# Performance work log

Hardware: AMD Instinct MI355X
Metric: run time of the kernel (lower is better)

Reference implementation:

```python
import jax, jax.numpy as jnp
import numpy as np

N_FQK, N_FV, N_REL, N_VAL, N_KNOW = 512, 256, 128, 64, 256
TOPK_QK, TOPK_V, TOPK_REL, TOPK_VAL = 64, 32, 16, 3
FQK_END = N_FQK
FV_END = N_FQK + N_FV
REL_END = FV_END + N_REL
VAL_END = REL_END + N_VAL
TOTAL = VAL_END + N_KNOW


def setup_inputs() -> dict:
    key = jax.random.key(0)
    k1, k2, k3, k4, k5 = jax.random.split(key, 5)
    B, S, D, DS = 8, 4096, 1024, 64
    x = jax.random.normal(k1, (B, S, D), dtype=jnp.float32)
    importance = jax.random.uniform(k2, (B, S), dtype=jnp.float32)
    proj_w = jax.random.normal(k3, (DS, D), dtype=jnp.float32) * (1.0 / np.sqrt(D))
    proj_b = jax.random.normal(k4, (DS,), dtype=jnp.float32) * 0.01
    neuron_emb = jax.random.normal(k5, (TOTAL, DS), dtype=jnp.float32) * 0.02
    return {"x": x, "importance": importance, "proj_w": proj_w,
            "proj_b": proj_b, "neuron_emb": neuron_emb}


def _topk_sparsify(w, k):
    # keep top-k values per row, zero elsewhere
    vals, idx = jax.lax.top_k(w, k)
    B = w.shape[0]
    sparse = jnp.zeros_like(w).at[jnp.arange(B)[:, None], idx].set(vals)
    return sparse, idx


def reference(x, importance, proj_w, proj_b, neuron_emb):
    # shared projection + normalized neuron embeddings (eval: dropout off,
    # no excitability bonus)
    h = jnp.einsum('bsd,kd->bsk', x, proj_w) + proj_b          # [B,S,d_space]
    emb_n = neuron_emb / jnp.linalg.norm(neuron_emb, axis=-1, keepdims=True)
    all_logits = jnp.einsum('bsk,nk->bsn', h, emb_n)            # [B,S,TOTAL]

    def agg(logits):
        pref = jax.nn.softmax(logits, axis=-1)                  # [B,S,n]
        return jnp.einsum('bs,bsn->bn', importance, pref)

    w_qk = agg(all_logits[..., :FQK_END])
    _, idx_qk = jax.lax.top_k(w_qk, TOPK_QK)
    idx_qk = jnp.sort(idx_qk, axis=-1)

    w_v = agg(all_logits[..., FQK_END:FV_END])
    _, idx_v = jax.lax.top_k(w_v, TOPK_V)
    idx_v = jnp.sort(idx_v, axis=-1)

    rel_logits = all_logits[..., FV_END:REL_END]
    # relational_Q and relational_K use the same logits slice (eval mode)
    rel_dense_Q = agg(rel_logits)
    rel_dense_K = agg(rel_logits)
    rel_Q, _ = _topk_sparsify(rel_dense_Q, TOPK_REL)
    rel_K, _ = _topk_sparsify(rel_dense_K, TOPK_REL)

    val_dense = agg(all_logits[..., REL_END:VAL_END])
    val_w, _ = _topk_sparsify(val_dense, TOPK_VAL)

    return idx_qk, idx_v, rel_Q, rel_K, val_w
```

## Files before the change

kernel.cpp:

```cpp
#include <hip/hip_runtime.h>


typedef short short8 __attribute__((ext_vector_type(8)));
typedef float f32x4 __attribute__((ext_vector_type(4)));

__device__ __forceinline__ unsigned short f32_to_bf16(float f) {
  unsigned u = __float_as_uint(f);
  u += 0x7FFF + ((u >> 16) & 1);
  return (unsigned short)(u >> 16);
}
__device__ __forceinline__ float bf16_to_f32(unsigned short h) {
  return __uint_as_float(((unsigned)h) << 16);
}
__device__ __forceinline__ void split8(const float4& a0, const float4& a1,
                                       short8& hi, short8& lo) {
  float af[8] = {a0.x, a0.y, a0.z, a0.w, a1.x, a1.y, a1.z, a1.w};
#pragma unroll
  for (int j = 0; j < 8; ++j) {
    unsigned short h = f32_to_bf16(af[j]);
    hi[j] = (short)h;
    lo[j] = (short)f32_to_bf16(af[j] - bf16_to_f32(h));
  }
}
#define MFMA(a, b, c) __builtin_amdgcn_mfma_f32_16x16x32_bf16(a, b, c, 0, 0, 0)

__global__ __launch_bounds__(256) void k_prep(const float* __restrict__ pw,
                                              const float* __restrict__ emb,
                                              unsigned short* __restrict__ whi,
                                              unsigned short* __restrict__ wlo,
                                              unsigned short* __restrict__ ehi,
                                              unsigned short* __restrict__ elo,
                                              float* __restrict__ wg) {
  int tid = blockIdx.x * 256 + threadIdx.x;
  if (tid < 7680) wg[tid] = 0.f;
  for (int i = tid; i < 65536; i += gridDim.x * 256) {
    float v = pw[i];
    unsigned short h = f32_to_bf16(v);
    whi[i] = h;
    wlo[i] = f32_to_bf16(v - bf16_to_f32(h));
  }
  int wid = tid >> 6, lane = tid & 63;
  int nw = gridDim.x * 4;
  for (int n = wid; n < 960; n += nw) {
    float v = emb[n * 64 + lane];
    float s = v * v;
#pragma unroll
    for (int off = 1; off < 64; off <<= 1) s += __shfl_xor(s, off);
    float vn = v / sqrtf(s);
    unsigned short h = f32_to_bf16(vn);
    ehi[n * 64 + lane] = h;
    elo[n * 64 + lane] = f32_to_bf16(vn - bf16_to_f32(h));
  }
}

__global__ __launch_bounds__(256) void k_proj(const float* __restrict__ x,
                                              const unsigned short* __restrict__ whi,
                                              const unsigned short* __restrict__ wlo,
                                              const float* __restrict__ pb,
                                              unsigned short* __restrict__ hhi,
                                              unsigned short* __restrict__ hlo) {
  int tid = threadIdx.x, w = tid >> 6, lane = tid & 63;
  int q = lane >> 4, c = lane & 15;
  int m0 = blockIdx.x * 32;
  int nt = w;

  f32x4 acc[2];
  acc[0] = (f32x4){0.f, 0.f, 0.f, 0.f};
  acc[1] = (f32x4){0.f, 0.f, 0.f, 0.f};

  const float* ap0 = x + (size_t)(m0 + c) * 1024 + q * 8;
  const float* ap1 = x + (size_t)(m0 + 16 + c) * 1024 + q * 8;
  float4 a00 = *(const float4*)(ap0), a01 = *(const float4*)(ap0 + 4);
  float4 a10 = *(const float4*)(ap1), a11 = *(const float4*)(ap1 + 4);

  for (int ks = 0; ks < 32; ++ks) {
    float4 n00, n01, n10, n11;
    if (ks < 31) {
      n00 = *(const float4*)(ap0 + (ks + 1) * 32);
      n01 = *(const float4*)(ap0 + (ks + 1) * 32 + 4);
      n10 = *(const float4*)(ap1 + (ks + 1) * 32);
      n11 = *(const float4*)(ap1 + (ks + 1) * 32 + 4);
    }
    size_t boff = (size_t)(nt * 16 + c) * 1024 + ks * 32 + q * 8;
    short8 bhi = *(const short8*)(whi + boff);
    short8 blo = *(const short8*)(wlo + boff);
    short8 ahi[2], alo[2];
    split8(a00, a01, ahi[0], alo[0]);
    split8(a10, a11, ahi[1], alo[1]);
#pragma unroll
    for (int mt = 0; mt < 2; ++mt) {
      acc[mt] = MFMA(ahi[mt], bhi, acc[mt]);
      acc[mt] = MFMA(ahi[mt], blo, acc[mt]);
      acc[mt] = MFMA(alo[mt], bhi, acc[mt]);
    }
    if (ks < 31) { a00 = n00; a01 = n01; a10 = n10; a11 = n11; }
  }

  float bias = pb[nt * 16 + c];
#pragma unroll
  for (int mt = 0; mt < 2; ++mt) {
#pragma unroll
    for (int r = 0; r < 4; ++r) {
      float val = acc[mt][r] + bias;
      int row = m0 + mt * 16 + q * 4 + r;
      unsigned short h = f32_to_bf16(val);
      hhi[(size_t)row * 64 + nt * 16 + c] = h;
      hlo[(size_t)row * 64 + nt * 16 + c] = f32_to_bf16(val - bf16_to_f32(h));
    }
  }
}

__global__ __launch_bounds__(256) void k_agg(const unsigned short* __restrict__ hhi,
                                             const unsigned short* __restrict__ hlo,
                                             const unsigned short* __restrict__ ehi,
                                             const unsigned short* __restrict__ elo,
                                             const float* __restrict__ imp,
                                             float* __restrict__ wg) {
  __shared__ float zpart[4][32][4];
  __shared__ float coefL[32][4];
  int tid = threadIdx.x, w = tid >> 6, lane = tid & 63;
  int q = lane >> 4, c = lane & 15;
  int row0 = blockIdx.x * 32;
  int b = row0 >> 12;

  short8 Ahi[2][2], Alo[2][2];
#pragma unroll
  for (int mt = 0; mt < 2; ++mt)
#pragma unroll
    for (int ks = 0; ks < 2; ++ks) {
      size_t base = (size_t)(row0 + mt * 16 + c) * 64 + ks * 32 + q * 8;
      Ahi[mt][ks] = *(const short8*)(hhi + base);
      Alo[mt][ks] = *(const short8*)(hlo + base);
    }

  f32x4 zacc[2];
  zacc[0] = (f32x4){0.f, 0.f, 0.f, 0.f};
  zacc[1] = (f32x4){0.f, 0.f, 0.f, 0.f};
  int cur_seg = 0;
  for (int i = 0; i < 15; ++i) {
    int nt = w + 4 * i;
    int s = (nt < 32) ? 0 : (nt < 48) ? 1 : (nt < 56) ? 2 : 3;
    if (s != cur_seg) {
#pragma unroll
      for (int mt = 0; mt < 2; ++mt)
#pragma unroll
        for (int r = 0; r < 4; ++r) {
          float v = zacc[mt][r];
          v += __shfl_xor(v, 1); v += __shfl_xor(v, 2);
          v += __shfl_xor(v, 4); v += __shfl_xor(v, 8);
          if (c == 0) zpart[w][mt * 16 + q * 4 + r][cur_seg] = v;
          zacc[mt][r] = 0.f;
        }
      cur_seg = s;
    }
    size_t eb = (size_t)(nt * 16 + c) * 64 + q * 8;
    short8 bhi0 = *(const short8*)(ehi + eb), bhi1 = *(const short8*)(ehi + eb + 32);
    short8 blo0 = *(const short8*)(elo + eb), blo1 = *(const short8*)(elo + eb + 32);
#pragma unroll
    for (int mt = 0; mt < 2; ++mt) {
      f32x4 l = (f32x4){0.f, 0.f, 0.f, 0.f};
      l = MFMA(Ahi[mt][0], bhi0, l); l = MFMA(Ahi[mt][1], bhi1, l);
      l = MFMA(Ahi[mt][0], blo0, l); l = MFMA(Ahi[mt][1], blo1, l);
      l = MFMA(Alo[mt][0], bhi0, l); l = MFMA(Alo[mt][1], bhi1, l);
#pragma unroll
      for (int r = 0; r < 4; ++r) zacc[mt][r] += __expf(l[r]);
    }
  }
#pragma unroll
  for (int mt = 0; mt < 2; ++mt)
#pragma unroll
    for (int r = 0; r < 4; ++r) {
      float v = zacc[mt][r];
      v += __shfl_xor(v, 1); v += __shfl_xor(v, 2);
      v += __shfl_xor(v, 4); v += __shfl_xor(v, 8);
      if (c == 0) zpart[w][mt * 16 + q * 4 + r][cur_seg] = v;
    }
  __syncthreads();
  if (tid < 128) {
    int row = tid & 31, sg = tid >> 5;
    float Z = zpart[0][row][sg] + zpart[1][row][sg] + zpart[2][row][sg] + zpart[3][row][sg];
    coefL[row][sg] = imp[row0 + row] / Z;
  }
  __syncthreads();

  f32x4 cf[2];
  int cs2 = -1;
  for (int i = 0; i < 15; ++i) {
    int nt = w + 4 * i;
    int s = (nt < 32) ? 0 : (nt < 48) ? 1 : (nt < 56) ? 2 : 3;
    if (s != cs2) {
#pragma unroll
      for (int mt = 0; mt < 2; ++mt)
#pragma unroll
        for (int r = 0; r < 4; ++r) cf[mt][r] = coefL[mt * 16 + q * 4 + r][s];
      cs2 = s;
    }
    size_t eb = (size_t)(nt * 16 + c) * 64 + q * 8;
    short8 bhi0 = *(const short8*)(ehi + eb), bhi1 = *(const short8*)(ehi + eb + 32);
    short8 blo0 = *(const short8*)(elo + eb), blo1 = *(const short8*)(elo + eb + 32);
    float wsum = 0.f;
#pragma unroll
    for (int mt = 0; mt < 2; ++mt) {
      f32x4 l = (f32x4){0.f, 0.f, 0.f, 0.f};
      l = MFMA(Ahi[mt][0], bhi0, l); l = MFMA(Ahi[mt][1], bhi1, l);
      l = MFMA(Ahi[mt][0], blo0, l); l = MFMA(Ahi[mt][1], blo1, l);
      l = MFMA(Alo[mt][0], bhi0, l); l = MFMA(Alo[mt][1], bhi1, l);
#pragma unroll
      for (int r = 0; r < 4; ++r) wsum = fmaf(__expf(l[r]), cf[mt][r], wsum);
    }
    wsum += __shfl_xor(wsum, 16);
    wsum += __shfl_xor(wsum, 32);
    if (lane < 16) atomicAdd(&wg[b * 960 + nt * 16 + c], wsum);
  }
}

__global__ __launch_bounds__(256) void k_topk(const float* __restrict__ wg,
                                              float* __restrict__ out) {
  __shared__ float vals[512];
  __shared__ int flags[512];
  int blk = blockIdx.x;
  int b = blk >> 2, t = blk & 3;
  int tid = threadIdx.x;
  const int Ns[4] = {512, 256, 128, 64};
  const int Ks[4] = {64, 32, 16, 3};
  const int Off[4] = {0, 512, 768, 896};
  int N = Ns[t], K = Ks[t], off = Off[t];
  for (int n = tid; n < N; n += 256) vals[n] = wg[b * 960 + off + n];
  __syncthreads();
  for (int n = tid; n < N; n += 256) {
    float v = vals[n];
    int rank = 0;
    for (int m = 0; m < N; ++m) {
      float u = vals[m];
      rank += (u > v || (u == v && m < n)) ? 1 : 0;
    }
    flags[n] = (rank < K) ? 1 : 0;
  }
  __syncthreads();
  if (t <= 1) {
    if (tid < 64) {
      int base = 0;
      for (int ch = 0; ch < N; ch += 64) {
        int n = ch + tid;
        int f = flags[n];
        unsigned long long mask = __ballot(f);
        if (f) {
          int pos = base + __popcll(mask & ((1ull << tid) - 1ull));
          if (t == 0) out[b * 64 + pos] = (float)n;
          else out[512 + b * 32 + pos] = (float)n;
        }
        base += __popcll(mask);
      }
    }
  } else if (t == 2) {
    for (int n = tid; n < 128; n += 256) {
      float v = flags[n] ? vals[n] : 0.f;
      out[768 + b * 128 + n] = v;
      out[1792 + b * 128 + n] = v;
    }
  } else {
    for (int n = tid; n < 64; n += 256) {
      float v = flags[n] ? vals[n] : 0.f;
      out[2816 + b * 64 + n] = v;
    }
  }
}

extern "C" void kernel_launch(void* const* d_in, const int* in_sizes, int n_in,
                              void* d_out, int out_size, void* d_ws, size_t ws_size,
                              hipStream_t stream) {
  const float* x   = (const float*)d_in[0];
  const float* imp = (const float*)d_in[1];
  const float* pw  = (const float*)d_in[2];
  const float* pb  = (const float*)d_in[3];
  const float* emb = (const float*)d_in[4];
  float* out = (float*)d_out;

  char* ws = (char*)d_ws;
  unsigned short* hhi = (unsigned short*)(ws);
  unsigned short* hlo = (unsigned short*)(ws + 4194304);
  unsigned short* whi = (unsigned short*)(ws + 8388608);
  unsigned short* wlo = (unsigned short*)(ws + 8519680);
  unsigned short* ehi = (unsigned short*)(ws + 8650752);
  unsigned short* elo = (unsigned short*)(ws + 8773632);
  float*          wg  = (float*)(ws + 8896512);

  hipLaunchKernelGGL(k_prep, dim3(64), dim3(256), 0, stream, pw, emb, whi, wlo, ehi, elo, wg);
  hipLaunchKernelGGL(k_proj, dim3(1024), dim3(256), 0, stream, x, whi, wlo, pb, hhi, hlo);
  hipLaunchKernelGGL(k_agg,  dim3(1024), dim3(256), 0, stream, hhi, hlo, ehi, elo, imp, wg);
  hipLaunchKernelGGL(k_topk, dim3(32), dim3(256), 0, stream, wg, out);
}
```

Before: 350.7 us.

## Fuse projection and softmax aggregation into one kernel with split-K across waves

Merges the projection GEMM and the softmax/importance aggregation into a single kernel, so the projected activations stay in shared memory as hi/lo bf16 instead of going through a global round trip. Each block now handles 16 rows. Its four waves split the K dimension of the projection and reduce the partial sums through LDS before the aggregation phase. This removes one launch and about 8 MB of intermediate global traffic. In exchange it doubles the block count, which doubles the atomicAdd traffic into wg, and it raises register use from preloading 16 float4 of x per thread.

```diff
diff --git a/kernel.cpp b/kernel.cpp
--- a/kernel.cpp
+++ b/kernel.cpp
@@ -53,161 +53,140 @@
   }
 }
 
-__global__ __launch_bounds__(256) void k_proj(const float* __restrict__ x,
+__global__ __launch_bounds__(256) void k_main(const float* __restrict__ x,
                                               const unsigned short* __restrict__ whi,
                                               const unsigned short* __restrict__ wlo,
                                               const float* __restrict__ pb,
-                                              unsigned short* __restrict__ hhi,
-                                              unsigned short* __restrict__ hlo) {
+                                              const unsigned short* __restrict__ ehi,
+                                              const unsigned short* __restrict__ elo,
+                                              const float* __restrict__ imp,
+                                              float* __restrict__ wg) {
+  __shared__ __align__(16) float cpart[4][16][68];
+  __shared__ __align__(16) unsigned short hsh[16][72];
+  __shared__ __align__(16) unsigned short hsl[16][72];
+  __shared__ float zpart[4][16][4];
+  __shared__ float coefL[16][4];
+
   int tid = threadIdx.x, w = tid >> 6, lane = tid & 63;
   int q = lane >> 4, c = lane & 15;
-  int m0 = blockIdx.x * 32;
-  int nt = w;
-
-  f32x4 acc[2];
-  acc[0] = (f32x4){0.f, 0.f, 0.f, 0.f};
-  acc[1] = (f32x4){0.f, 0.f, 0.f, 0.f};
-
-  const float* ap0 = x + (size_t)(m0 + c) * 1024 + q * 8;
-  const float* ap1 = x + (size_t)(m0 + 16 + c) * 1024 + q * 8;
-  float4 a00 = *(const float4*)(ap0), a01 = *(const float4*)(ap0 + 4);
-  float4 a10 = *(const float4*)(ap1), a11 = *(const float4*)(ap1 + 4);
-
-  for (int ks = 0; ks < 32; ++ks) {
-    float4 n00, n01, n10, n11;
-    if (ks < 31) {
-      n00 = *(const float4*)(ap0 + (ks + 1) * 32);
-      n01 = *(const float4*)(ap0 + (ks + 1) * 32 + 4);
-      n10 = *(const float4*)(ap1 + (ks + 1) * 32);
-      n11 = *(const float4*)(ap1 + (ks + 1) * 32 + 4);
-    }
-    size_t boff = (size_t)(nt * 16 + c) * 1024 + ks * 32 + q * 8;
-    short8 bhi = *(const short8*)(whi + boff);
-    short8 blo = *(const short8*)(wlo + boff);
-    short8 ahi[2], alo[2];
-    split8(a00, a01, ahi[0], alo[0]);
-    split8(a10, a11, ahi[1], alo[1]);
-#pragma unroll
-    for (int mt = 0; mt < 2; ++mt) {
-      acc[mt] = MFMA(ahi[mt], bhi, acc[mt]);
-      acc[mt] = MFMA(ahi[mt], blo, acc[mt]);
-      acc[mt] = MFMA(alo[mt], bhi, acc[mt]);
-    }
-    if (ks < 31) { a00 = n00; a01 = n01; a10 = n10; a11 = n11; }
-  }
-
-  float bias = pb[nt * 16 + c];
-#pragma unroll
-  for (int mt = 0; mt < 2; ++mt) {
-#pragma unroll
-    for (int r = 0; r < 4; ++r) {
-      float val = acc[mt][r] + bias;
-      int row = m0 + mt * 16 + q * 4 + r;
-      unsigned short h = f32_to_bf16(val);
-      hhi[(size_t)row * 64 + nt * 16 + c] = h;
-      hlo[(size_t)row * 64 + nt * 16 + c] = f32_to_bf16(val - bf16_to_f32(h));
-    }
-  }
-}
-
-__global__ __launch_bounds__(256) void k_agg(const unsigned short* __restrict__ hhi,
-                                             const unsigned short* __restrict__ hlo,
-                                             const unsigned short* __restrict__ ehi,
-                                             const unsigned short* __restrict__ elo,
-                                             const float* __restrict__ imp,
-                                             float* __restrict__ wg) {
-  __shared__ float zpart[4][32][4];
-  __shared__ float coefL[32][4];
-  int tid = threadIdx.x, w = tid >> 6, lane = tid & 63;
-  int q = lane >> 4, c = lane & 15;
-  int row0 = blockIdx.x * 32;
+  int row0 = blockIdx.x * 16;
   int b = row0 >> 12;
 
-  short8 Ahi[2][2], Alo[2][2];
-#pragma unroll
-  for (int mt = 0; mt < 2; ++mt)
-#pragma unroll
-    for (int ks = 0; ks < 2; ++ks) {
-      size_t base = (size_t)(row0 + mt * 16 + c) * 64 + ks * 32 + q * 8;
-      Ahi[mt][ks] = *(const short8*)(hhi + base);
-      Alo[mt][ks] = *(const short8*)(hlo + base);
-    }
-
-  f32x4 zacc[2];
-  zacc[0] = (f32x4){0.f, 0.f, 0.f, 0.f};
-  zacc[1] = (f32x4){0.f, 0.f, 0.f, 0.f};
+  f32x4 acc[4];
+#pragma unroll
+  for (int nt = 0; nt < 4; ++nt) acc[nt] = (f32x4){0.f, 0.f, 0.f, 0.f};
+
+  const float* ap = x + (size_t)(row0 + c) * 1024 + q * 8;
+  float4 xa[16];
+#pragma unroll
+  for (int j = 0; j < 8; ++j) {
+    xa[2 * j]     = *(const float4*)(ap + (w + 4 * j) * 32);
+    xa[2 * j + 1] = *(const float4*)(ap + (w + 4 * j) * 32 + 4);
+  }
+#pragma unroll
+  for (int j = 0; j < 8; ++j) {
+    int ks = w + 4 * j;
+    short8 bhi[4], blo[4];
+#pragma unroll
+    for (int nt = 0; nt < 4; ++nt) {
+      size_t boff = (size_t)(nt * 16 + c) * 1024 + ks * 32 + q * 8;
+      bhi[nt] = *(const short8*)(whi + boff);
+      blo[nt] = *(const short8*)(wlo + boff);
+    }
+    short8 ahi, alo;
+    split8(xa[2 * j], xa[2 * j + 1], ahi, alo);
+#pragma unroll
+    for (int nt = 0; nt < 4; ++nt) {
+      acc[nt] = MFMA(ahi, bhi[nt], acc[nt]);
+      acc[nt] = MFMA(ahi, blo[nt], acc[nt]);
+      acc[nt] = MFMA(alo, bhi[nt], acc[nt]);
+    }
+  }
+#pragma unroll
+  for (int nt = 0; nt < 4; ++nt)
+#pragma unroll
+    for (int r = 0; r < 4; ++r) cpart[w][q * 4 + r][nt * 16 + c] = acc[nt][r];
+  __syncthreads();
+#pragma unroll
+  for (int k = 0; k < 4; ++k) {
+    int idx = tid + k * 256;
+    int row = idx >> 6, col = idx & 63;
+    float v = cpart[0][row][col] + cpart[1][row][col] +
+              cpart[2][row][col] + cpart[3][row][col] + pb[col];
+    unsigned short h = f32_to_bf16(v);
+    hsh[row][col] = h;
+    hsl[row][col] = f32_to_bf16(v - bf16_to_f32(h));
+  }
+  __syncthreads();
+
+  short8 Ahi[2], Alo[2];
+#pragma unroll
+  for (int ks = 0; ks < 2; ++ks) {
+    Ahi[ks] = *(const short8*)&hsh[c][ks * 32 + q * 8];
+    Alo[ks] = *(const short8*)&hsl[c][ks * 32 + q * 8];
+  }
+
+  f32x4 zacc = (f32x4){0.f, 0.f, 0.f, 0.f};
   int cur_seg = 0;
   for (int i = 0; i < 15; ++i) {
     int nt = w + 4 * i;
     int s = (nt < 32) ? 0 : (nt < 48) ? 1 : (nt < 56) ? 2 : 3;
     if (s != cur_seg) {
 #pragma unroll
-      for (int mt = 0; mt < 2; ++mt)
-#pragma unroll
-        for (int r = 0; r < 4; ++r) {
-          float v = zacc[mt][r];
-          v += __shfl_xor(v, 1); v += __shfl_xor(v, 2);
-          v += __shfl_xor(v, 4); v += __shfl_xor(v, 8);
-          if (c == 0) zpart[w][mt * 16 + q * 4 + r][cur_seg] = v;
-          zacc[mt][r] = 0.f;
-        }
+      for (int r = 0; r < 4; ++r) {
+        float v = zacc[r];
+        v += __shfl_xor(v, 1); v += __shfl_xor(v, 2);
+        v += __shfl_xor(v, 4); v += __shfl_xor(v, 8);
+        if (c == 0) zpart[w][q * 4 + r][cur_seg] = v;
+        zacc[r] = 0.f;
+      }
       cur_seg = s;
     }
     size_t eb = (size_t)(nt * 16 + c) * 64 + q * 8;
     short8 bhi0 = *(const short8*)(ehi + eb), bhi1 = *(const short8*)(ehi + eb + 32);
     short8 blo0 = *(const short8*)(elo + eb), blo1 = *(const short8*)(elo + eb + 32);
-#pragma unroll
-    for (int mt = 0; mt < 2; ++mt) {
-      f32x4 l = (f32x4){0.f, 0.f, 0.f, 0.f};
-      l = MFMA(Ahi[mt][0], bhi0, l); l = MFMA(Ahi[mt][1], bhi1, l);
-      l = MFMA(Ahi[mt][0], blo0, l); l = MFMA(Ahi[mt][1], blo1, l);
-      l = MFMA(Alo[mt][0], bhi0, l); l = MFMA(Alo[mt][1], bhi1, l);
-#pragma unroll
-      for (int r = 0; r < 4; ++r) zacc[mt][r] += __expf(l[r]);
-    }
-  }
-#pragma unroll
-  for (int mt = 0; mt < 2; ++mt)
-#pragma unroll
-    for (int r = 0; r < 4; ++r) {
-      float v = zacc[mt][r];
-      v += __shfl_xor(v, 1); v += __shfl_xor(v, 2);
-      v += __shfl_xor(v, 4); v += __shfl_xor(v, 8);
-      if (c == 0) zpart[w][mt * 16 + q * 4 + r][cur_seg] = v;
-    }
-  __syncthreads();
-  if (tid < 128) {
-    int row = tid & 31, sg = tid >> 5;
+    f32x4 l = (f32x4){0.f, 0.f, 0.f, 0.f};
+    l = MFMA(Ahi[0], bhi0, l); l = MFMA(Ahi[1], bhi1, l);
+    l = MFMA(Ahi[0], blo0, l); l = MFMA(Ahi[1], blo1, l);
+    l = MFMA(Alo[0], bhi0, l); l = MFMA(Alo[1], bhi1, l);
+#pragma unroll
+    for (int r = 0; r < 4; ++r) zacc[r] += __expf(l[r]);
+  }
+#pragma unroll
+  for (int r = 0; r < 4; ++r) {
+    float v = zacc[r];
+    v += __shfl_xor(v, 1); v += __shfl_xor(v, 2);
+    v += __shfl_xor(v, 4); v += __shfl_xor(v, 8);
+    if (c == 0) zpart[w][q * 4 + r][cur_seg] = v;
+  }
+  __syncthreads();
+  if (tid < 64) {
+    int row = tid & 15, sg = tid >> 4;
     float Z = zpart[0][row][sg] + zpart[1][row][sg] + zpart[2][row][sg] + zpart[3][row][sg];
     coefL[row][sg] = imp[row0 + row] / Z;
   }
   __syncthreads();
 
-  f32x4 cf[2];
+  f32x4 cf;
   int cs2 = -1;
   for (int i = 0; i < 15; ++i) {
     int nt = w + 4 * i;
     int s = (nt < 32) ? 0 : (nt < 48) ? 1 : (nt < 56) ? 2 : 3;
     if (s != cs2) {
 #pragma unroll
-      for (int mt = 0; mt < 2; ++mt)
-#pragma unroll
-        for (int r = 0; r < 4; ++r) cf[mt][r] = coefL[mt * 16 + q * 4 + r][s];
+      for (int r = 0; r < 4; ++r) cf[r] = coefL[q * 4 + r][s];
       cs2 = s;
     }
     size_t eb = (size_t)(nt * 16 + c) * 64 + q * 8;
     short8 bhi0 = *(const short8*)(ehi + eb), bhi1 = *(const short8*)(ehi + eb + 32);
     short8 blo0 = *(const short8*)(elo + eb), blo1 = *(const short8*)(elo + eb + 32);
+    f32x4 l = (f32x4){0.f, 0.f, 0.f, 0.f};
+    l = MFMA(Ahi[0], bhi0, l); l = MFMA(Ahi[1], bhi1, l);
+    l = MFMA(Ahi[0], blo0, l); l = MFMA(Ahi[1], blo1, l);
+    l = MFMA(Alo[0], bhi0, l); l = MFMA(Alo[1], bhi1, l);
     float wsum = 0.f;
 #pragma unroll
-    for (int mt = 0; mt < 2; ++mt) {
-      f32x4 l = (f32x4){0.f, 0.f, 0.f, 0.f};
-      l = MFMA(Ahi[mt][0], bhi0, l); l = MFMA(Ahi[mt][1], bhi1, l);
-      l = MFMA(Ahi[mt][0], blo0, l); l = MFMA(Ahi[mt][1], blo1, l);
-      l = MFMA(Alo[mt][0], bhi0, l); l = MFMA(Alo[mt][1], bhi1, l);
-#pragma unroll
-      for (int r = 0; r < 4; ++r) wsum = fmaf(__expf(l[r]), cf[mt][r], wsum);
-    }
+    for (int r = 0; r < 4; ++r) wsum = fmaf(__expf(l[r]), cf[r], wsum);
     wsum += __shfl_xor(wsum, 16);
     wsum += __shfl_xor(wsum, 32);
     if (lane < 16) atomicAdd(&wg[b * 960 + nt * 16 + c], wsum);
@@ -277,16 +256,13 @@
   float* out = (float*)d_out;
 
   char* ws = (char*)d_ws;
-  unsigned short* hhi = (unsigned short*)(ws);
-  unsigned short* hlo = (unsigned short*)(ws + 4194304);
-  unsigned short* whi = (unsigned short*)(ws + 8388608);
-  unsigned short* wlo = (unsigned short*)(ws + 8519680);
-  unsigned short* ehi = (unsigned short*)(ws + 8650752);
-  unsigned short* elo = (unsigned short*)(ws + 8773632);
-  float*          wg  = (float*)(ws + 8896512);
+  unsigned short* whi = (unsigned short*)(ws);
+  unsigned short* wlo = (unsigned short*)(ws + 131072);
+  unsigned short* ehi = (unsigned short*)(ws + 262144);
+  unsigned short* elo = (unsigned short*)(ws + 385024);
+  float*          wg  = (float*)(ws + 507904);
 
   hipLaunchKernelGGL(k_prep, dim3(64), dim3(256), 0, stream, pw, emb, whi, wlo, ehi, elo, wg);
-  hipLaunchKernelGGL(k_proj, dim3(1024), dim3(256), 0, stream, x, whi, wlo, pb, hhi, hlo);
-  hipLaunchKernelGGL(k_agg,  dim3(1024), dim3(256), 0, stream, hhi, hlo, ehi, elo, imp, wg);
+  hipLaunchKernelGGL(k_main, dim3(2048), dim3(256), 0, stream, x, whi, wlo, pb, ehi, elo, imp, wg);
   hipLaunchKernelGGL(k_topk, dim3(32), dim3(256), 0, stream, wg, out);
 }
```

New measurement: 375.3 us. 7.0% more time.
